# Performance work log

Measured on AMD Instinct MI355X. Metric: run time of the kernel, lower is better.

Reference implementation:

```python
import jax, jax.numpy as jnp
import numpy as np

B, S, E, H = 4, 2048, 1024, 16
D = E // H  # head_size = 64


def setup_inputs() -> dict:
    key = jax.random.key(0)
    ks = jax.random.split(key, 5)
    x = jax.random.normal(ks[0], (B, S, E), dtype=jnp.float32)
    # nn.Linear default init ~ U(-1/sqrt(fan_in), 1/sqrt(fan_in))
    bound = 1.0 / np.sqrt(E)
    W_qkv = jax.random.uniform(ks[1], (E, 3 * E), dtype=jnp.float32, minval=-bound, maxval=bound)
    b_qkv = jax.random.uniform(ks[2], (3 * E,), dtype=jnp.float32, minval=-bound, maxval=bound)
    W_out = jax.random.uniform(ks[3], (E, E), dtype=jnp.float32, minval=-bound, maxval=bound)
    b_out = jax.random.uniform(ks[4], (E,), dtype=jnp.float32, minval=-bound, maxval=bound)
    return {"x": x, "W_qkv": W_qkv, "b_qkv": b_qkv, "W_out": W_out, "b_out": b_out, "mask": 1}


def reference(x, W_qkv, b_qkv, W_out, b_out, mask):
    qkv = x @ W_qkv + b_qkv                              # [B,S,3E]
    qkv = qkv.reshape(B, S, H, 3 * D).transpose(0, 2, 1, 3)  # [B,H,S,3D]
    q, k, v = jnp.split(qkv, 3, axis=-1)                  # each [B,H,S,D]
    scale = 1.0 / np.sqrt(E)  # NOTE: original divides by sqrt(n_embd), not sqrt(head_size)
    y = jnp.einsum('bhqd,bhkd->bhqk', q, k) * scale       # [B,H,S,S]
    if mask:
        causal = jnp.tril(jnp.ones((S, S), dtype=bool))
        y = jnp.where(causal, y, -1e9)
    y = jax.nn.softmax(y, axis=-1)
    vals = jnp.einsum('bhqk,bhkd->bhqd', y, v)            # [B,H,S,D]
    vals = vals.transpose(0, 2, 1, 3).reshape(B, S, E)
    return vals @ W_out + b_out
```

## Files before the change

kernel.cpp:

```cpp
#include <hip/hip_runtime.h>
#include <hip/hip_bf16.h>
#include <cstdint>
#include <cstddef>

typedef __bf16 bf16;
typedef __bf16 bf16x8 __attribute__((ext_vector_type(8)));
typedef float f32x4 __attribute__((ext_vector_type(4)));
typedef unsigned int u32x4 __attribute__((ext_vector_type(4)));
typedef unsigned int u32x2 __attribute__((ext_vector_type(2)));

#define DEVINL __device__ __forceinline__

namespace {
constexpr int Bb = 4, Ss = 2048, Ee = 1024, Hh = 16;
constexpr int Mm = Bb * Ss;
constexpr int N_QKV = 3 * Ee;
}

DEVINL void gl_lds16(const bf16* g, bf16* l) {
  __builtin_amdgcn_global_load_lds((const __attribute__((address_space(1))) void*)g,
                                   (__attribute__((address_space(3))) void*)l, 16, 0, 0);
}

DEVINL unsigned int pkbf(float a, float b) {
  bf16 x = (bf16)a, y = (bf16)b;
  return (unsigned int)__builtin_bit_cast(unsigned short, x) |
         ((unsigned int)__builtin_bit_cast(unsigned short, y) << 16);
}


__global__ void k_cvt_bf16(const float* __restrict__ in, bf16* __restrict__ out, int n) {
  int i = (blockIdx.x * 256 + threadIdx.x) * 8;
  if (i >= n) return;
  float4 a = *(const float4*)(in + i);
  float4 c = *(const float4*)(in + i + 4);
  bf16x8 v = {(bf16)a.x, (bf16)a.y, (bf16)a.z, (bf16)a.w,
              (bf16)c.x, (bf16)c.y, (bf16)c.z, (bf16)c.w};
  *(bf16x8*)(out + i) = v;
}

__global__ void k_transpose_cvt(const float* __restrict__ in, bf16* __restrict__ out, int R, int C) {
  __shared__ float tile[32][33];
  const int c0 = blockIdx.x * 32, r0 = blockIdx.y * 32;
  const int tx = threadIdx.x, ty = threadIdx.y;
  for (int i = 0; i < 32; i += 8)
    tile[ty + i][tx] = in[(size_t)(r0 + ty + i) * C + (c0 + tx)];
  __syncthreads();
  for (int i = 0; i < 32; i += 8)
    out[(size_t)(c0 + ty + i) * R + (r0 + tx)] = (bf16)tile[tx][ty + i];
}

__global__ void k_vt(const bf16* __restrict__ qkvb, bf16* __restrict__ vt) {
  __shared__ bf16 t[32][33];
  const int bh = blockIdx.z;
  const int b = bh >> 4, h = bh & 15;
  const int s0 = blockIdx.x * 32, d0 = blockIdx.y * 32;
  const int tx = threadIdx.x, ty = threadIdx.y;
  const bf16* src = qkvb + (size_t)b * Ss * N_QKV + h * 192 + 128;
  for (int i = 0; i < 32; i += 8)
    t[ty + i][tx] = src[(size_t)(s0 + ty + i) * N_QKV + d0 + tx];
  __syncthreads();
  bf16* dst = vt + ((size_t)bh * 64 + d0) * Ss + s0;
  for (int i = 0; i < 32; i += 8)
    dst[(size_t)(ty + i) * Ss + tx] = t[tx][ty + i];
}


__global__ __launch_bounds__(256) void k_qkv_gemm(const bf16* __restrict__ A,
                                                  const bf16* __restrict__ Bt,
                                                  const float* __restrict__ bias,
                                                  bf16* __restrict__ out) {
  __shared__ bf16 sm[2 * 128 * 64];
  bf16* As = sm;
  bf16* Bs = sm + 128 * 64;
  const int tid = threadIdx.x, wid = tid >> 6, lane = tid & 63;
  const int wm = wid >> 1, wn = wid & 1;
  const int fr = lane & 15, kg = lane >> 4;
  const int m0 = blockIdx.y * 128, n0 = blockIdx.x * 128;
  const int K = Ee;

  f32x4 acc[4][4] = {};

  const int ar = wid * 32 + (lane >> 3);
  const int ac = (lane & 7) * 8;
  const bf16* Ag = A + (size_t)(m0 + ar) * K + ac;
  const bf16* Bg = Bt + (size_t)(n0 + ar) * K + ac;
  bf16* AsW = As + wid * 32 * 64;
  bf16* BsW = Bs + wid * 32 * 64;

  for (int kt = 0; kt < K; kt += 64) {
    __syncthreads();
    for (int i = 0; i < 4; ++i) {
      gl_lds16(Ag + (size_t)(i * 8) * K + kt, AsW + i * 8 * 64);
      gl_lds16(Bg + (size_t)(i * 8) * K + kt, BsW + i * 8 * 64);
    }
    __syncthreads();
    for (int kk = 0; kk < 2; ++kk) {
      bf16x8 af[4], bfr[4];
      for (int mi = 0; mi < 4; ++mi)
        af[mi] = *(const bf16x8*)(As + (wm * 64 + mi * 16 + fr) * 64 + kk * 32 + kg * 8);
      for (int ni = 0; ni < 4; ++ni)
        bfr[ni] = *(const bf16x8*)(Bs + (wn * 64 + ni * 16 + fr) * 64 + kk * 32 + kg * 8);
      for (int mi = 0; mi < 4; ++mi)
        for (int ni = 0; ni < 4; ++ni)
          acc[mi][ni] = __builtin_amdgcn_mfma_f32_16x16x32_bf16(af[mi], bfr[ni], acc[mi][ni], 0, 0, 0);
    }
  }
  for (int ni = 0; ni < 4; ++ni) {
    const int col = n0 + wn * 64 + ni * 16 + fr;
    const float bv = bias[col];
    for (int mi = 0; mi < 4; ++mi) {
      const int mbase = m0 + wm * 64 + mi * 16 + kg * 4;
      for (int r = 0; r < 4; ++r)
        out[(size_t)(mbase + r) * N_QKV + col] = (bf16)(acc[mi][ni][r] + bv);
    }
  }
}

__global__ __launch_bounds__(256) void k_out_gemm(const bf16* __restrict__ A,
                                                  const bf16* __restrict__ Bt,
                                                  const float* __restrict__ bias,
                                                  float* __restrict__ out) {
  __shared__ bf16 sm[2 * 128 * 64];
  bf16* As = sm;
  bf16* Bs = sm + 128 * 64;
  const int tid = threadIdx.x, wid = tid >> 6, lane = tid & 63;
  const int wm = wid >> 1, wn = wid & 1;
  const int fr = lane & 15, kg = lane >> 4;
  const int m0 = blockIdx.y * 128, n0 = blockIdx.x * 128;
  const int K = Ee;

  f32x4 acc[4][4] = {};

  const int ar = wid * 32 + (lane >> 3);
  const int ac = (lane & 7) * 8;
  const bf16* Ag = A + (size_t)(m0 + ar) * K + ac;
  const bf16* Bg = Bt + (size_t)(n0 + ar) * K + ac;
  bf16* AsW = As + wid * 32 * 64;
  bf16* BsW = Bs + wid * 32 * 64;

  for (int kt = 0; kt < K; kt += 64) {
    __syncthreads();
    for (int i = 0; i < 4; ++i) {
      gl_lds16(Ag + (size_t)(i * 8) * K + kt, AsW + i * 8 * 64);
      gl_lds16(Bg + (size_t)(i * 8) * K + kt, BsW + i * 8 * 64);
    }
    __syncthreads();
    for (int kk = 0; kk < 2; ++kk) {
      bf16x8 af[4], bfr[4];
      for (int mi = 0; mi < 4; ++mi)
        af[mi] = *(const bf16x8*)(As + (wm * 64 + mi * 16 + fr) * 64 + kk * 32 + kg * 8);
      for (int ni = 0; ni < 4; ++ni)
        bfr[ni] = *(const bf16x8*)(Bs + (wn * 64 + ni * 16 + fr) * 64 + kk * 32 + kg * 8);
      for (int mi = 0; mi < 4; ++mi)
        for (int ni = 0; ni < 4; ++ni)
          acc[mi][ni] = __builtin_amdgcn_mfma_f32_16x16x32_bf16(af[mi], bfr[ni], acc[mi][ni], 0, 0, 0);
    }
  }
  for (int ni = 0; ni < 4; ++ni) {
    const int col = n0 + wn * 64 + ni * 16 + fr;
    const float bv = bias[col];
    for (int mi = 0; mi < 4; ++mi) {
      const int mbase = m0 + wm * 64 + mi * 16 + kg * 4;
      for (int r = 0; r < 4; ++r)
        out[(size_t)(mbase + r) * Ee + col] = acc[mi][ni][r] + bv;
    }
  }
}


__global__ __launch_bounds__(256, 3) void k_attn(const bf16* __restrict__ qkv,
                                                 const bf16* __restrict__ vt,
                                                 bf16* __restrict__ vals) {
  constexpr float SC = 0.03125f * 1.44269504f;
  const int g = blockIdx.x;
  const int qt = 15 - (g >> 6);
  const int bh = g & 63;
  const int b = bh >> 4, h = bh & 15;
  const int q0 = qt * 128;
  const int tid = threadIdx.x, w = tid >> 6, lane = tid & 63;
  const int fr = lane & 15, kg = lane >> 4;
  const int rl = lane >> 3, cl = (lane & 7) ^ (lane >> 3);

  __shared__ bf16 KsB[2][4096];
  __shared__ bf16 VtB[2][4096];

  const bf16* base = qkv + (size_t)b * Ss * N_QKV + h * 192;
  const bf16* kb = base + 64 + (size_t)rl * N_QKV + cl * 8;
  const bf16* vb = vt + (size_t)(b * Hh + h) * 64 * Ss + (size_t)rl * Ss + cl * 8;

  const int gA = (kg & 1) * 32 + fr;
  const int gB = gA + 16;
  const bool hiSel = (kg >> 1) != 0;

  bf16x8 aq[2][2];
  for (int sub = 0; sub < 2; ++sub) {
    const bf16* qr = base + (size_t)(q0 + w * 32 + sub * 16 + fr) * N_QKV + kg * 8;
    aq[sub][0] = *(const bf16x8*)(qr);
    aq[sub][1] = *(const bf16x8*)(qr + 32);
  }

  float m_run[2] = {-1e30f, -1e30f}, l_run[2] = {0.f, 0.f};
  f32x4 o_acc[2][4] = {};

  const int nt = 2 * qt + 2;

  for (int t = 0; t < 2; ++t) {
    const int i = w * 2 + t;
    gl_lds16(kb + (size_t)(i * 8) * N_QKV, KsB[0] + i * 512);
    gl_lds16(vb + (size_t)(i * 8) * Ss, VtB[0] + i * 512);
  }

  int cur = 0;
  for (int it = 0; it < nt; ++it) {
    const int kv0 = it * 64;
    __syncthreads();
    if (it + 1 < nt) {
      const int kvn = kv0 + 64;
      for (int t = 0; t < 2; ++t) {
        const int i = w * 2 + t;
        gl_lds16(kb + (size_t)(kvn + i * 8) * N_QKV, KsB[cur ^ 1] + i * 512);
        gl_lds16(vb + (size_t)(i * 8) * Ss + kvn, VtB[cur ^ 1] + i * 512);
      }
    }
    const bool active = (kv0 <= q0 + w * 32 + 31);
    if (active) {
      f32x4 sacc[2][4] = {};
      for (int kk = 0; kk < 2; ++kk) {
        bf16x8 bk[4];
        for (int ni = 0; ni < 4; ++ni) {
          const int rb = ni * 16 + fr;
          bk[ni] = *(const bf16x8*)(KsB[cur] + rb * 64 + (((kk * 4 + kg) ^ (rb & 7)) * 8));
        }
        __builtin_amdgcn_s_setprio(1);
        for (int sub = 0; sub < 2; ++sub)
          for (int ni = 0; ni < 4; ++ni)
            sacc[sub][ni] =
                __builtin_amdgcn_mfma_f32_16x16x32_bf16(bk[ni], aq[sub][kk], sacc[sub][ni], 0, 0, 0);
        __builtin_amdgcn_s_setprio(0);
      }
      bf16x8 bp[2][2];
      for (int sub = 0; sub < 2; ++sub) {
        const int qs = q0 + w * 32 + sub * 16;
        float p[4][4];
        float mnew = -1e30f;
        if (kv0 + 63 > qs) {
          const int q = qs + fr;
          for (int ni = 0; ni < 4; ++ni)
            for (int r = 0; r < 4; ++r) {
              const int k = kv0 + ni * 16 + kg * 4 + r;
              float s = sacc[sub][ni][r] * SC;
              if (k > q) s = -1e30f;
              p[ni][r] = s;
              mnew = fmaxf(mnew, s);
            }
        } else {
          for (int ni = 0; ni < 4; ++ni)
            for (int r = 0; r < 4; ++r) {
              float s = sacc[sub][ni][r] * SC;
              p[ni][r] = s;
              mnew = fmaxf(mnew, s);
            }
        }
        mnew = fmaxf(mnew, __shfl_xor(mnew, 16, 64));
        mnew = fmaxf(mnew, __shfl_xor(mnew, 32, 64));
        const float mn = fmaxf(m_run[sub], mnew);
        const float fs = exp2f(m_run[sub] - mn);
        m_run[sub] = mn;
        float rs = 0.f;
        for (int ni = 0; ni < 4; ++ni)
          for (int r = 0; r < 4; ++r) {
            const float e = exp2f(p[ni][r] - mn);
            p[ni][r] = e;
            rs += e;
          }
        rs += __shfl_xor(rs, 16, 64);
        rs += __shfl_xor(rs, 32, 64);
        l_run[sub] = l_run[sub] * fs + rs;
        for (int ni = 0; ni < 4; ++ni)
          for (int r = 0; r < 4; ++r)
            o_acc[sub][ni][r] *= fs;
        unsigned int Wlo[4], Whi[4];
        for (int ni = 0; ni < 4; ++ni) {
          Wlo[ni] = pkbf(p[ni][0], p[ni][1]);
          Whi[ni] = pkbf(p[ni][2], p[ni][3]);
        }
        for (int kk = 0; kk < 2; ++kk) {
          const int i0 = 2 * kk, i1 = 2 * kk + 1;
          unsigned int a0 = (unsigned int)__shfl((int)Wlo[i0], gA, 64);
          unsigned int a1 = (unsigned int)__shfl((int)Wlo[i1], gA, 64);
          unsigned int b0 = (unsigned int)__shfl((int)Whi[i0], gA, 64);
          unsigned int b1 = (unsigned int)__shfl((int)Whi[i1], gA, 64);
          unsigned int c0 = (unsigned int)__shfl((int)Wlo[i0], gB, 64);
          unsigned int c1 = (unsigned int)__shfl((int)Wlo[i1], gB, 64);
          unsigned int d0 = (unsigned int)__shfl((int)Whi[i0], gB, 64);
          unsigned int d1 = (unsigned int)__shfl((int)Whi[i1], gB, 64);
          u32x4 wv = {hiSel ? a1 : a0, hiSel ? b1 : b0, hiSel ? c1 : c0, hiSel ? d1 : d0};
          bp[sub][kk] = __builtin_bit_cast(bf16x8, wv);
        }
      }
      for (int kk = 0; kk < 2; ++kk) {
        bf16x8 bv[4];
        for (int ni = 0; ni < 4; ++ni) {
          const int rb = ni * 16 + fr;
          bv[ni] = *(const bf16x8*)(VtB[cur] + rb * 64 + (((kk * 4 + kg) ^ (rb & 7)) * 8));
        }
        __builtin_amdgcn_s_setprio(1);
        for (int sub = 0; sub < 2; ++sub)
          for (int ni = 0; ni < 4; ++ni)
            o_acc[sub][ni] =
                __builtin_amdgcn_mfma_f32_16x16x32_bf16(bv[ni], bp[sub][kk], o_acc[sub][ni], 0, 0, 0);
        __builtin_amdgcn_s_setprio(0);
      }
    }
    cur ^= 1;
  }

  for (int sub = 0; sub < 2; ++sub) {
    const float inv = 1.f / l_run[sub];
    const int q = q0 + w * 32 + sub * 16 + fr;
    bf16* dst = vals + ((size_t)b * Ss + q) * Ee + h * 64 + kg * 4;
    for (int ni = 0; ni < 4; ++ni) {
      u32x2 pk2 = {pkbf(o_acc[sub][ni][0] * inv, o_acc[sub][ni][1] * inv),
                   pkbf(o_acc[sub][ni][2] * inv, o_acc[sub][ni][3] * inv)};
      *(u32x2*)(dst + ni * 16) = pk2;
    }
  }
}


extern "C" void kernel_launch(void* const* d_in, const int* in_sizes, int n_in,
                              void* d_out, int out_size, void* d_ws, size_t ws_size,
                              hipStream_t stream) {
  const float* x    = (const float*)d_in[0];
  const float* Wqkv = (const float*)d_in[1];
  const float* bqkv = (const float*)d_in[2];
  const float* Wout = (const float*)d_in[3];
  const float* bout = (const float*)d_in[4];
  float* out = (float*)d_out;

  char* ws = (char*)d_ws;
  bf16* x_bf  = (bf16*)(ws);
  bf16* vt    = (bf16*)(ws);
  bf16* WqkvT = (bf16*)(ws + (size_t)16777216);
  bf16* WoutT = (bf16*)(ws + (size_t)16777216 + 6291456);
  bf16* qkvb  = (bf16*)(ws + (size_t)25165824);
  bf16* valsb = (bf16*)(ws + (size_t)75497472);

  k_cvt_bf16<<<dim3(Mm * Ee / 2048), dim3(256), 0, stream>>>(x, x_bf, Mm * Ee);
  k_transpose_cvt<<<dim3(N_QKV / 32, Ee / 32), dim3(32, 8), 0, stream>>>(Wqkv, WqkvT, Ee, N_QKV);
  k_transpose_cvt<<<dim3(Ee / 32, Ee / 32), dim3(32, 8), 0, stream>>>(Wout, WoutT, Ee, Ee);
  k_qkv_gemm<<<dim3(N_QKV / 128, Mm / 128), dim3(256), 0, stream>>>(x_bf, WqkvT, bqkv, qkvb);
  k_vt<<<dim3(Ss / 32, 2, Bb * Hh), dim3(32, 8), 0, stream>>>(qkvb, vt);
  k_attn<<<dim3(Ss / 128 * Hh * Bb), dim3(256), 0, stream>>>(qkvb, vt, valsb);
  k_out_gemm<<<dim3(Ee / 128, Mm / 128), dim3(256), 0, stream>>>(valsb, WoutT, bout, out);
}
```

Before: 223.8 us.

## Fuse Q/K/V head split and V transpose into QKV GEMM epilogue, lazy softmax rescale

The QKV GEMM epilogue now writes Q (pre-scaled by the softmax scale times log2e), K in per-head contiguous [bh,S,64] layout, and V transposed directly. This removes the separate k_vt transpose kernel and the strided qkv reads in attention. The attention kernel drops the per-score scale multiply and skips the running-max rescale of o_acc and l unless the new max exceeds the old by more than 8. It also raises the occupancy hint to 4 blocks. The V writes from the epilogue are 8-byte scattered stores and the Q/K stores are 2-byte strided, and the lazy rescale relies on fp32 headroom.

Result: slower. 228.3 us (+2.0%).

```diff
diff --git a/kernel.cpp b/kernel.cpp
--- a/kernel.cpp
+++ b/kernel.cpp
@@ -15,6 +15,7 @@
 constexpr int Bb = 4, Ss = 2048, Ee = 1024, Hh = 16;
 constexpr int Mm = Bb * Ss;
 constexpr int N_QKV = 3 * Ee;
+constexpr float SCQ = 0.03125f * 1.44269504f;
 }
 
 DEVINL void gl_lds16(const bf16* g, bf16* l) {
@@ -50,26 +51,13 @@
     out[(size_t)(c0 + ty + i) * R + (r0 + tx)] = (bf16)tile[tx][ty + i];
 }
 
-__global__ void k_vt(const bf16* __restrict__ qkvb, bf16* __restrict__ vt) {
-  __shared__ bf16 t[32][33];
-  const int bh = blockIdx.z;
-  const int b = bh >> 4, h = bh & 15;
-  const int s0 = blockIdx.x * 32, d0 = blockIdx.y * 32;
-  const int tx = threadIdx.x, ty = threadIdx.y;
-  const bf16* src = qkvb + (size_t)b * Ss * N_QKV + h * 192 + 128;
-  for (int i = 0; i < 32; i += 8)
-    t[ty + i][tx] = src[(size_t)(s0 + ty + i) * N_QKV + d0 + tx];
-  __syncthreads();
-  bf16* dst = vt + ((size_t)bh * 64 + d0) * Ss + s0;
-  for (int i = 0; i < 32; i += 8)
-    dst[(size_t)(ty + i) * Ss + tx] = t[tx][ty + i];
-}
-
 
 __global__ __launch_bounds__(256) void k_qkv_gemm(const bf16* __restrict__ A,
                                                   const bf16* __restrict__ Bt,
                                                   const float* __restrict__ bias,
-                                                  bf16* __restrict__ out) {
+                                                  bf16* __restrict__ qbuf,
+                                                  bf16* __restrict__ kbuf,
+                                                  bf16* __restrict__ vtb) {
   __shared__ bf16 sm[2 * 128 * 64];
   bf16* As = sm;
   bf16* Bs = sm + 128 * 64;
@@ -106,13 +94,30 @@
           acc[mi][ni] = __builtin_amdgcn_mfma_f32_16x16x32_bf16(af[mi], bfr[ni], acc[mi][ni], 0, 0, 0);
     }
   }
+  const int row_b = m0 >> 11;
+  const int s_base = (m0 & 2047) + wm * 64;
   for (int ni = 0; ni < 4; ++ni) {
-    const int col = n0 + wn * 64 + ni * 16 + fr;
-    const float bv = bias[col];
-    for (int mi = 0; mi < 4; ++mi) {
-      const int mbase = m0 + wm * 64 + mi * 16 + kg * 4;
-      for (int r = 0; r < 4; ++r)
-        out[(size_t)(mbase + r) * N_QKV + col] = (bf16)(acc[mi][ni][r] + bv);
+    const int col0 = n0 + wn * 64 + ni * 16;
+    const int h = col0 / 192;
+    const int w192 = col0 - h * 192;
+    const int cls = w192 >> 6;
+    const float bv = bias[col0 + fr];
+    if (cls == 2) {
+      const int d = w192 - 128 + fr;
+      bf16* dst = vtb + (((size_t)row_b * Hh + h) * 64 + d) * Ss + s_base;
+      for (int mi = 0; mi < 4; ++mi) {
+        u32x2 pk2 = {pkbf(acc[mi][ni][0] + bv, acc[mi][ni][1] + bv),
+                     pkbf(acc[mi][ni][2] + bv, acc[mi][ni][3] + bv)};
+        *(u32x2*)(dst + mi * 16 + kg * 4) = pk2;
+      }
+    } else {
+      bf16* buf = (cls == 0) ? qbuf : kbuf;
+      const float sc = (cls == 0) ? SCQ : 1.f;
+      const int d = (w192 & 63) + fr;
+      bf16* dst = buf + (((size_t)row_b * Hh + h) * Ss + s_base) * 64 + d;
+      for (int mi = 0; mi < 4; ++mi)
+        for (int r = 0; r < 4; ++r)
+          dst[(size_t)(mi * 16 + kg * 4 + r) * 64] = (bf16)((acc[mi][ni][r] + bv) * sc);
     }
   }
 }
@@ -169,10 +174,10 @@
 }
 
 
-__global__ __launch_bounds__(256, 3) void k_attn(const bf16* __restrict__ qkv,
-                                                 const bf16* __restrict__ vt,
+__global__ __launch_bounds__(256, 4) void k_attn(const bf16* __restrict__ qbuf,
+                                                 const bf16* __restrict__ kbuf,
+                                                 const bf16* __restrict__ vtb,
                                                  bf16* __restrict__ vals) {
-  constexpr float SC = 0.03125f * 1.44269504f;
   const int g = blockIdx.x;
   const int qt = 15 - (g >> 6);
   const int bh = g & 63;
@@ -185,9 +190,9 @@
   __shared__ bf16 KsB[2][4096];
   __shared__ bf16 VtB[2][4096];
 
-  const bf16* base = qkv + (size_t)b * Ss * N_QKV + h * 192;
-  const bf16* kb = base + 64 + (size_t)rl * N_QKV + cl * 8;
-  const bf16* vb = vt + (size_t)(b * Hh + h) * 64 * Ss + (size_t)rl * Ss + cl * 8;
+  const bf16* qb = qbuf + (size_t)bh * Ss * 64;
+  const bf16* kb = kbuf + (size_t)bh * Ss * 64 + (size_t)rl * 64 + cl * 8;
+  const bf16* vb = vtb + (size_t)bh * 64 * Ss + (size_t)rl * Ss + cl * 8;
 
   const int gA = (kg & 1) * 32 + fr;
   const int gB = gA + 16;
@@ -195,7 +200,7 @@
 
   bf16x8 aq[2][2];
   for (int sub = 0; sub < 2; ++sub) {
-    const bf16* qr = base + (size_t)(q0 + w * 32 + sub * 16 + fr) * N_QKV + kg * 8;
+    const bf16* qr = qb + (size_t)(q0 + w * 32 + sub * 16 + fr) * 64 + kg * 8;
     aq[sub][0] = *(const bf16x8*)(qr);
     aq[sub][1] = *(const bf16x8*)(qr + 32);
   }
@@ -207,7 +212,7 @@
 
   for (int t = 0; t < 2; ++t) {
     const int i = w * 2 + t;
-    gl_lds16(kb + (size_t)(i * 8) * N_QKV, KsB[0] + i * 512);
+    gl_lds16(kb + (size_t)(i * 8) * 64, KsB[0] + i * 512);
     gl_lds16(vb + (size_t)(i * 8) * Ss, VtB[0] + i * 512);
   }
 
@@ -219,7 +224,7 @@
       const int kvn = kv0 + 64;
       for (int t = 0; t < 2; ++t) {
         const int i = w * 2 + t;
-        gl_lds16(kb + (size_t)(kvn + i * 8) * N_QKV, KsB[cur ^ 1] + i * 512);
+        gl_lds16(kb + (size_t)(kvn + i * 8) * 64, KsB[cur ^ 1] + i * 512);
         gl_lds16(vb + (size_t)(i * 8) * Ss + kvn, VtB[cur ^ 1] + i * 512);
       }
     }
@@ -249,7 +254,7 @@
           for (int ni = 0; ni < 4; ++ni)
             for (int r = 0; r < 4; ++r) {
               const int k = kv0 + ni * 16 + kg * 4 + r;
-              float s = sacc[sub][ni][r] * SC;
+              float s = sacc[sub][ni][r];
               if (k > q) s = -1e30f;
               p[ni][r] = s;
               mnew = fmaxf(mnew, s);
@@ -257,16 +262,25 @@
         } else {
           for (int ni = 0; ni < 4; ++ni)
             for (int r = 0; r < 4; ++r) {
-              float s = sacc[sub][ni][r] * SC;
+              float s = sacc[sub][ni][r];
               p[ni][r] = s;
               mnew = fmaxf(mnew, s);
             }
         }
         mnew = fmaxf(mnew, __shfl_xor(mnew, 16, 64));
         mnew = fmaxf(mnew, __shfl_xor(mnew, 32, 64));
-        const float mn = fmaxf(m_run[sub], mnew);
-        const float fs = exp2f(m_run[sub] - mn);
-        m_run[sub] = mn;
+        float mn;
+        if (__all(mnew - m_run[sub] <= 8.f)) {
+          mn = m_run[sub];
+        } else {
+          mn = fmaxf(m_run[sub], mnew);
+          const float fs = exp2f(m_run[sub] - mn);
+          m_run[sub] = mn;
+          l_run[sub] *= fs;
+          for (int ni = 0; ni < 4; ++ni)
+            for (int r = 0; r < 4; ++r)
+              o_acc[sub][ni][r] *= fs;
+        }
         float rs = 0.f;
         for (int ni = 0; ni < 4; ++ni)
           for (int r = 0; r < 4; ++r) {
@@ -276,10 +290,7 @@
           }
         rs += __shfl_xor(rs, 16, 64);
         rs += __shfl_xor(rs, 32, 64);
-        l_run[sub] = l_run[sub] * fs + rs;
-        for (int ni = 0; ni < 4; ++ni)
-          for (int r = 0; r < 4; ++r)
-            o_acc[sub][ni][r] *= fs;
+        l_run[sub] += rs;
         unsigned int Wlo[4], Whi[4];
         for (int ni = 0; ni < 4; ++ni) {
           Wlo[ni] = pkbf(p[ni][0], p[ni][1]);
@@ -340,18 +351,19 @@
   float* out = (float*)d_out;
 
   char* ws = (char*)d_ws;
+  const size_t MiB = 1048576;
   bf16* x_bf  = (bf16*)(ws);
-  bf16* vt    = (bf16*)(ws);
-  bf16* WqkvT = (bf16*)(ws + (size_t)16777216);
-  bf16* WoutT = (bf16*)(ws + (size_t)16777216 + 6291456);
-  bf16* qkvb  = (bf16*)(ws + (size_t)25165824);
-  bf16* valsb = (bf16*)(ws + (size_t)75497472);
+  bf16* WqkvT = (bf16*)(ws + 16 * MiB);
+  bf16* WoutT = (bf16*)(ws + 22 * MiB);
+  bf16* qbuf  = (bf16*)(ws + 24 * MiB);
+  bf16* kbuf  = (bf16*)(ws + 40 * MiB);
+  bf16* vtb   = (bf16*)(ws + 56 * MiB);
+  bf16* valsb = (bf16*)(ws + 72 * MiB);
 
   k_cvt_bf16<<<dim3(Mm * Ee / 2048), dim3(256), 0, stream>>>(x, x_bf, Mm * Ee);
   k_transpose_cvt<<<dim3(N_QKV / 32, Ee / 32), dim3(32, 8), 0, stream>>>(Wqkv, WqkvT, Ee, N_QKV);
   k_transpose_cvt<<<dim3(Ee / 32, Ee / 32), dim3(32, 8), 0, stream>>>(Wout, WoutT, Ee, Ee);
-  k_qkv_gemm<<<dim3(N_QKV / 128, Mm / 128), dim3(256), 0, stream>>>(x_bf, WqkvT, bqkv, qkvb);
-  k_vt<<<dim3(Ss / 32, 2, Bb * Hh), dim3(32, 8), 0, stream>>>(qkvb, vt);
-  k_attn<<<dim3(Ss / 128 * Hh * Bb), dim3(256), 0, stream>>>(qkvb, vt, valsb);
+  k_qkv_gemm<<<dim3(N_QKV / 128, Mm / 128), dim3(256), 0, stream>>>(x_bf, WqkvT, bqkv, qbuf, kbuf, vtb);
+  k_attn<<<dim3(Ss / 128 * Hh * Bb), dim3(256), 0, stream>>>(qbuf, kbuf, vtb, valsb);
   k_out_gemm<<<dim3(Ee / 128, Mm / 128), dim3(256), 0, stream>>>(valsb, WoutT, bout, out);
 }
```
